# Optimization experiments

Measured on AMD Instinct MI355X. Metric: run time of the kernel, lower is better.

Reference implementation:

```python
import jax, jax.numpy as jnp
import numpy as np

N = 50000   # nodes
E = 600000  # edges
D = 128     # node_features (EvolveGCNO in=out channels)
H = 128     # hidden_dim (final Linear out)


def setup_inputs() -> dict:
    key = jax.random.key(0)
    ks = jax.random.split(key, 9)
    stdv = 1.0 / np.sqrt(D)
    u = lambda k, shape: jax.random.uniform(k, shape, jnp.float32, -stdv, stdv)
    return {
        "x": jax.random.normal(ks[0], (N, D), jnp.float32),
        "edge_index": jax.random.randint(ks[1], (2, E), 0, N),
        "edge_weight": jax.random.uniform(ks[2], (E,), jnp.float32),
        "W0": u(ks[3], (D, D)),        # EvolveGCNO initial_weight (squeezed)
        "w_ih": u(ks[4], (3 * D, D)),  # GRU input weights (r|z|n)
        "w_hh": u(ks[5], (3 * D, D)),  # GRU hidden weights (r|z|n)
        "b_ih": u(ks[6], (3 * D,)),
        "b_hh": u(ks[7], (3 * D,)),
        "W_lin": u(ks[8], (H, D)),     # torch Linear weight [out, in]
        "b_lin": jnp.zeros((H,), jnp.float32),
    }


def _gru_step(x, h, w_ih, w_hh, b_ih, b_hh):
    # One torch.nn.GRU cell step; here x == h == W0 (weight evolution).
    gi = x @ w_ih.T + b_ih
    gh = h @ w_hh.T + b_hh
    i_r, i_z, i_n = jnp.split(gi, 3, axis=-1)
    h_r, h_z, h_n = jnp.split(gh, 3, axis=-1)
    r = jax.nn.sigmoid(i_r + h_r)
    z = jax.nn.sigmoid(i_z + h_z)
    n = jnp.tanh(i_n + r * h_n)
    return (1.0 - z) * n + z * h


def reference(x, edge_index, edge_weight, W0, w_ih, w_hh, b_ih, b_hh, W_lin, b_lin):
    # 1) Evolve the GCN weight with one GRU step (input = hidden = W0).
    W = _gru_step(W0, W0, w_ih, w_hh, b_ih, b_hh)  # [D, D]

    # 2) GCNConv_Fixed_W: add self-loops (weight 1), symmetric normalization.
    loops = jnp.arange(N)
    row = jnp.concatenate([edge_index[0], loops])  # source
    col = jnp.concatenate([edge_index[1], loops])  # target
    ew = jnp.concatenate([edge_weight, jnp.ones((N,), x.dtype)])
    deg = jax.ops.segment_sum(ew, col, num_segments=N)
    dinv = jnp.where(deg > 0, jax.lax.rsqrt(deg), 0.0)
    norm = dinv[row] * ew * dinv[col]  # [E+N]

    xw = x @ W                                        # [N, D]
    h = jax.ops.segment_sum(norm[:, None] * xw[row], col, num_segments=N)  # [N, D]

    # 3) ReLU + Linear
    h = jax.nn.relu(h)
    return h @ W_lin.T + b_lin  # [N, H]
```

## Files before the change

kernel.cpp:

```cpp
#include <hip/hip_runtime.h>
#include <hip/hip_bf16.h>

#define NN 50000
#define EE 600000
#define DD 128
#define CAP 48
#define CNT_SHIFT 25
#define SUM_MASK 0x1FFFFFFu

typedef __attribute__((ext_vector_type(8))) __bf16 bf16x8;
typedef __attribute__((ext_vector_type(8))) short short8;
typedef __attribute__((ext_vector_type(4))) float f32x4;

__device__ __forceinline__ unsigned short f2bf(float f) {
    union { float f; unsigned u; } c; c.f = f;
    unsigned r = (c.u + 0x7fffu + ((c.u >> 16) & 1u)) >> 16;
    return (unsigned short)r;
}
__device__ __forceinline__ float bflo(unsigned u) {
    union { unsigned u; float f; } c; c.u = u << 16; return c.f;
}
__device__ __forceinline__ float bfhi(unsigned u) {
    union { unsigned u; float f; } c; c.u = u & 0xffff0000u; return c.f;
}
__device__ __forceinline__ float degof(unsigned p) {
    return 1.0f + (float)(p & SUM_MASK) * (1.0f / 65536.0f);
}

__global__ __launch_bounds__(256) void init_kernel(
    unsigned* __restrict__ cnt32,
    const float* __restrict__ W0, const float* __restrict__ w_ih,
    const float* __restrict__ w_hh, const float* __restrict__ b_ih,
    const float* __restrict__ b_hh, unsigned short* __restrict__ Wbt,
    const float* __restrict__ x, short* __restrict__ xb)
{
    if (blockIdx.x >= 113) {
        int u = (blockIdx.x - 113) * 256 + threadIdx.x;
        if (u < NN * DD / 8) {
            const float4* p = (const float4*)x + (size_t)u * 2;
            float4 f0 = p[0], f1 = p[1];
            short8 v;
            v[0] = (short)f2bf(f0.x); v[1] = (short)f2bf(f0.y);
            v[2] = (short)f2bf(f0.z); v[3] = (short)f2bf(f0.w);
            v[4] = (short)f2bf(f1.x); v[5] = (short)f2bf(f1.y);
            v[6] = (short)f2bf(f1.z); v[7] = (short)f2bf(f1.w);
            *(short8*)(xb + (size_t)u * 8) = v;
        }
        return;
    }
    if (blockIdx.x < 49) {
        int i = blockIdx.x * 256 + threadIdx.x;
        if (i < 50176 * 4 / 16) ((uint4*)cnt32)[i] = make_uint4(0u, 0u, 0u, 0u);
        return;
    }
    int idx = (blockIdx.x - 49) * 256 + threadIdx.x;
    int i = idx >> 7, j = idx & 127;
    const float4* a  = (const float4*)(W0  + i * DD);
    const float4* pr = (const float4*)(w_ih + (j        ) * DD);
    const float4* pz = (const float4*)(w_ih + (j + 128  ) * DD);
    const float4* pn = (const float4*)(w_ih + (j + 256  ) * DD);
    const float4* qr = (const float4*)(w_hh + (j        ) * DD);
    const float4* qz = (const float4*)(w_hh + (j + 128  ) * DD);
    const float4* qn = (const float4*)(w_hh + (j + 256  ) * DD);
    float ir = 0.f, iz = 0.f, inn = 0.f, hr = 0.f, hz = 0.f, hn = 0.f;
    for (int d = 0; d < DD / 4; ++d) {
        float4 av = a[d];
        float4 t;
        t = pr[d]; ir  += av.x*t.x + av.y*t.y + av.z*t.z + av.w*t.w;
        t = pz[d]; iz  += av.x*t.x + av.y*t.y + av.z*t.z + av.w*t.w;
        t = pn[d]; inn += av.x*t.x + av.y*t.y + av.z*t.z + av.w*t.w;
        t = qr[d]; hr  += av.x*t.x + av.y*t.y + av.z*t.z + av.w*t.w;
        t = qz[d]; hz  += av.x*t.x + av.y*t.y + av.z*t.z + av.w*t.w;
        t = qn[d]; hn  += av.x*t.x + av.y*t.y + av.z*t.z + av.w*t.w;
    }
    ir += b_ih[j]; iz += b_ih[j + 128]; inn += b_ih[j + 256];
    hr += b_hh[j]; hz += b_hh[j + 128]; hn  += b_hh[j + 256];
    float r = 1.f / (1.f + expf(-(ir + hr)));
    float z = 1.f / (1.f + expf(-(iz + hz)));
    float n = tanhf(inn + r * hn);
    float w = (1.f - z) * n + z * W0[idx];
    Wbt[j * DD + i] = f2bf(w);
}

__global__ __launch_bounds__(256) void histfill_kernel(
    const int* __restrict__ row, const int* __restrict__ col,
    const float* __restrict__ ew,
    unsigned* __restrict__ cnt32, unsigned* __restrict__ edges)
{
    int e = blockIdx.x * 256 + threadIdx.x;
    if (e >= EE) return;
    int c = col[e];
    unsigned wq = (unsigned)(ew[e] * 65536.0f);
    if (wq > 65535u) wq = 65535u;
    unsigned old = atomicAdd(&cnt32[c], (1u << CNT_SHIFT) | wq);
    unsigned oldcnt = old >> CNT_SHIFT;
    if (oldcnt < CAP)
        edges[(size_t)c * CAP + oldcnt] = (unsigned)row[e] | (wq << 16);
}

__global__ __launch_bounds__(256) void gather_kernel(
    const unsigned* __restrict__ edges, const unsigned* __restrict__ cnt32,
    const unsigned* __restrict__ xbu, unsigned* __restrict__ aggu)
{
    int wid  = threadIdx.x >> 6;
    int lane = threadIdx.x & 63;
    int node = blockIdx.x * 4 + wid;
    if (node >= NN) return;
    unsigned pn = cnt32[node];
    int n = (int)(pn >> CNT_SHIFT); if (n > CAP) n = CAP;
    const unsigned* eb = edges + (size_t)node * CAP;
    float s = rsqrtf(degof(pn));
    unsigned xs = xbu[(size_t)node * 64 + lane];
    float ax = s * bflo(xs), ay = s * bfhi(xs);
    int k = 0;
    int n8 = n & ~7;
    for (; k < n8; k += 8) {
        uint4 ra = *(const uint4*)(eb + k);
        uint4 rb = *(const uint4*)(eb + k + 4);
        int s0 = (int)(ra.x & 0xFFFFu), s1 = (int)(ra.y & 0xFFFFu);
        int s2 = (int)(ra.z & 0xFFFFu), s3 = (int)(ra.w & 0xFFFFu);
        int s4 = (int)(rb.x & 0xFFFFu), s5 = (int)(rb.y & 0xFFFFu);
        int s6 = (int)(rb.z & 0xFFFFu), s7 = (int)(rb.w & 0xFFFFu);
        unsigned p0 = cnt32[s0], p1 = cnt32[s1], p2 = cnt32[s2], p3 = cnt32[s3];
        unsigned p4 = cnt32[s4], p5 = cnt32[s5], p6 = cnt32[s6], p7 = cnt32[s7];
        unsigned x0 = xbu[(size_t)s0 * 64 + lane];
        unsigned x1 = xbu[(size_t)s1 * 64 + lane];
        unsigned x2 = xbu[(size_t)s2 * 64 + lane];
        unsigned x3 = xbu[(size_t)s3 * 64 + lane];
        unsigned x4 = xbu[(size_t)s4 * 64 + lane];
        unsigned x5 = xbu[(size_t)s5 * 64 + lane];
        unsigned x6 = xbu[(size_t)s6 * 64 + lane];
        unsigned x7 = xbu[(size_t)s7 * 64 + lane];
        float v0 = (float)(ra.x >> 16) * (1.0f / 65536.0f) * rsqrtf(degof(p0));
        float v1 = (float)(ra.y >> 16) * (1.0f / 65536.0f) * rsqrtf(degof(p1));
        float v2 = (float)(ra.z >> 16) * (1.0f / 65536.0f) * rsqrtf(degof(p2));
        float v3 = (float)(ra.w >> 16) * (1.0f / 65536.0f) * rsqrtf(degof(p3));
        float v4 = (float)(rb.x >> 16) * (1.0f / 65536.0f) * rsqrtf(degof(p4));
        float v5 = (float)(rb.y >> 16) * (1.0f / 65536.0f) * rsqrtf(degof(p5));
        float v6 = (float)(rb.z >> 16) * (1.0f / 65536.0f) * rsqrtf(degof(p6));
        float v7 = (float)(rb.w >> 16) * (1.0f / 65536.0f) * rsqrtf(degof(p7));
        ax += v0 * bflo(x0) + v1 * bflo(x1) + v2 * bflo(x2) + v3 * bflo(x3)
            + v4 * bflo(x4) + v5 * bflo(x5) + v6 * bflo(x6) + v7 * bflo(x7);
        ay += v0 * bfhi(x0) + v1 * bfhi(x1) + v2 * bfhi(x2) + v3 * bfhi(x3)
            + v4 * bfhi(x4) + v5 * bfhi(x5) + v6 * bfhi(x6) + v7 * bfhi(x7);
    }
    int n4 = n & ~3;
    for (; k < n4; k += 4) {
        uint4 rc = *(const uint4*)(eb + k);
        int s0 = (int)(rc.x & 0xFFFFu), s1 = (int)(rc.y & 0xFFFFu);
        int s2 = (int)(rc.z & 0xFFFFu), s3 = (int)(rc.w & 0xFFFFu);
        unsigned p0 = cnt32[s0], p1 = cnt32[s1], p2 = cnt32[s2], p3 = cnt32[s3];
        unsigned x0 = xbu[(size_t)s0 * 64 + lane];
        unsigned x1 = xbu[(size_t)s1 * 64 + lane];
        unsigned x2 = xbu[(size_t)s2 * 64 + lane];
        unsigned x3 = xbu[(size_t)s3 * 64 + lane];
        float v0 = (float)(rc.x >> 16) * (1.0f / 65536.0f) * rsqrtf(degof(p0));
        float v1 = (float)(rc.y >> 16) * (1.0f / 65536.0f) * rsqrtf(degof(p1));
        float v2 = (float)(rc.z >> 16) * (1.0f / 65536.0f) * rsqrtf(degof(p2));
        float v3 = (float)(rc.w >> 16) * (1.0f / 65536.0f) * rsqrtf(degof(p3));
        ax += v0 * bflo(x0) + v1 * bflo(x1) + v2 * bflo(x2) + v3 * bflo(x3);
        ay += v0 * bfhi(x0) + v1 * bfhi(x1) + v2 * bfhi(x2) + v3 * bfhi(x3);
    }
    for (; k < n; ++k) {
        unsigned r0 = eb[k];
        int s0 = (int)(r0 & 0xFFFFu);
        unsigned p0 = cnt32[s0];
        unsigned x0 = xbu[(size_t)s0 * 64 + lane];
        float v0 = (float)(r0 >> 16) * (1.0f / 65536.0f) * rsqrtf(degof(p0));
        ax += v0 * bflo(x0); ay += v0 * bfhi(x0);
    }
    aggu[(size_t)node * 64 + lane] =
        (unsigned)f2bf(ax * s) | ((unsigned)f2bf(ay * s) << 16);
}

__global__ __launch_bounds__(256) void fused_gemm(
    const short* __restrict__ agg, const short* __restrict__ Wbt,
    const float* __restrict__ Wlin, const float* __restrict__ bias,
    float* __restrict__ out)
{
    __shared__ __align__(16) short Bs1[DD * DD];
    __shared__ __align__(16) short Bs2[DD * DD];
    __shared__ __align__(16) short As[64 * DD];
    const int t = threadIdx.x;
    const int i0 = blockIdx.x * 64;

    for (int u = t; u < 2048; u += 256) {
        int byte = u << 4;
        int brow = byte >> 8;
        *(short8*)((char*)Bs1 + (byte ^ ((brow & 7) << 4))) =
            *(const short8*)((const char*)Wbt + byte);
    }
    for (int u = t; u < 2048; u += 256) {
        int brow = u >> 4;
        int kc = (u & 15) << 3;
        const float4* p = (const float4*)(Wlin + brow * DD + kc);
        float4 f0 = p[0], f1 = p[1];
        short8 v;
        v[0] = (short)f2bf(f0.x); v[1] = (short)f2bf(f0.y);
        v[2] = (short)f2bf(f0.z); v[3] = (short)f2bf(f0.w);
        v[4] = (short)f2bf(f1.x); v[5] = (short)f2bf(f1.y);
        v[6] = (short)f2bf(f1.z); v[7] = (short)f2bf(f1.w);
        int byte = (brow << 8) + (kc << 1);
        *(short8*)((char*)Bs2 + (byte ^ ((brow & 7) << 4))) = v;
    }
    for (int u = t; u < 1024; u += 256) {
        int arow = u >> 4;
        int kc = (u & 15) << 3;
        int grow = i0 + arow;
        short8 v;
#pragma unroll
        for (int i = 0; i < 8; ++i) v[i] = 0;
        if (grow < NN)
            v = *(const short8*)(agg + (size_t)grow * DD + kc);
        int byte = (arow << 8) + (kc << 1);
        *(short8*)((char*)As + (byte ^ ((arow & 7) << 4))) = v;
    }
    __syncthreads();

    const int lane = t & 63, wv = t >> 6;
    const int c0 = lane & 15, g = lane >> 4;
    const int arow = wv * 16 + c0;
    f32x4 acc[8];
#pragma unroll
    for (int n = 0; n < 8; ++n) { acc[n][0] = acc[n][1] = acc[n][2] = acc[n][3] = 0.f; }

#pragma unroll
    for (int s = 0; s < 4; ++s) {
        int k0 = s * 32 + g * 8;
        int abyte = (arow << 8) + (k0 << 1);
        bf16x8 a = *(const bf16x8*)((const char*)As + (abyte ^ ((arow & 7) << 4)));
#pragma unroll
        for (int n = 0; n < 8; ++n) {
            int bcol = n * 16 + c0;
            int bbyte = (bcol << 8) + (k0 << 1);
            bf16x8 b = *(const bf16x8*)((const char*)Bs1 + (bbyte ^ ((bcol & 7) << 4)));
            acc[n] = __builtin_amdgcn_mfma_f32_16x16x32_bf16(a, b, acc[n], 0, 0, 0);
        }
    }
    __syncthreads();

#pragma unroll
    for (int n = 0; n < 8; ++n) {
        int ccol = n * 16 + c0;
#pragma unroll
        for (int r = 0; r < 4; ++r) {
            int hrow = wv * 16 + g * 4 + r;
            int byte = (hrow << 8) + (ccol << 1);
            *(unsigned short*)((char*)As + (byte ^ ((hrow & 7) << 4))) =
                f2bf(fmaxf(acc[n][r], 0.f));
        }
    }
    __syncthreads();

#pragma unroll
    for (int n = 0; n < 8; ++n) { acc[n][0] = acc[n][1] = acc[n][2] = acc[n][3] = 0.f; }

#pragma unroll
    for (int s = 0; s < 4; ++s) {
        int k0 = s * 32 + g * 8;
        int abyte = (arow << 8) + (k0 << 1);
        bf16x8 a = *(const bf16x8*)((const char*)As + (abyte ^ ((arow & 7) << 4)));
#pragma unroll
        for (int n = 0; n < 8; ++n) {
            int bcol = n * 16 + c0;
            int bbyte = (bcol << 8) + (k0 << 1);
            bf16x8 b = *(const bf16x8*)((const char*)Bs2 + (bbyte ^ ((bcol & 7) << 4)));
            acc[n] = __builtin_amdgcn_mfma_f32_16x16x32_bf16(a, b, acc[n], 0, 0, 0);
        }
    }

#pragma unroll
    for (int n = 0; n < 8; ++n) {
        int ccol = n * 16 + c0;
        float bb = bias[ccol];
#pragma unroll
        for (int r = 0; r < 4; ++r) {
            int grow = i0 + wv * 16 + g * 4 + r;
            if (grow < NN)
                out[(size_t)grow * DD + ccol] = acc[n][r] + bb;
        }
    }
}

extern "C" void kernel_launch(void* const* d_in, const int* in_sizes, int n_in,
                              void* d_out, int out_size, void* d_ws, size_t ws_size,
                              hipStream_t stream)
{
    const float* x    = (const float*)d_in[0];
    const int*   ei   = (const int*)d_in[1];
    const float* ew   = (const float*)d_in[2];
    const float* W0   = (const float*)d_in[3];
    const float* w_ih = (const float*)d_in[4];
    const float* w_hh = (const float*)d_in[5];
    const float* b_ih = (const float*)d_in[6];
    const float* b_hh = (const float*)d_in[7];
    const float* Wlin = (const float*)d_in[8];
    const float* blin = (const float*)d_in[9];
    float* out = (float*)d_out;

    const int* row = ei;
    const int* col = ei + EE;

    char* ws = (char*)d_ws;
    unsigned short* Wbt = (unsigned short*)ws;
    unsigned* cnt32 = (unsigned*)(ws + 32768);
    short* xb   = (short*)(ws + 233472);
    short* agg  = (short*)(ws + 13033472);
    unsigned* edges = (unsigned*)(ws + 25833472);

    init_kernel<<<3238, 256, 0, stream>>>(cnt32, W0, w_ih, w_hh, b_ih, b_hh, Wbt, x, xb);

    histfill_kernel<<<(EE + 255) / 256, 256, 0, stream>>>(row, col, ew, cnt32, edges);

    gather_kernel<<<(NN + 3) / 4, 256, 0, stream>>>(
        edges, cnt32, (const unsigned*)xb, (unsigned*)agg);

    fused_gemm<<<(NN + 63) / 64, 256, 0, stream>>>(
        agg, (const short*)Wbt, Wlin, blin, out);
}
```

Measured before the change: 121.2 us.

## Fuse neighbor gather into the GEMM kernel via shared memory

Merges the gather aggregation kernel into the fused GEMM: each wave aggregates 16 nodes directly into the shared-memory A tile instead of writing an intermediate bf16 buffer to global memory. This removes the intermediate write/read and one kernel launch. In exchange the latency-bound gather now runs at much lower occupancy (few large-LDS blocks, serial nodes per wave), which may reduce latency hiding.

Result: slower. 174.3 us (+43.8%).

```diff
diff --git a/kernel.cpp b/kernel.cpp
--- a/kernel.cpp
+++ b/kernel.cpp
@@ -98,83 +98,9 @@
         edges[(size_t)c * CAP + oldcnt] = (unsigned)row[e] | (wq << 16);
 }
 
-__global__ __launch_bounds__(256) void gather_kernel(
+__global__ __launch_bounds__(256) void gather_gemm(
     const unsigned* __restrict__ edges, const unsigned* __restrict__ cnt32,
-    const unsigned* __restrict__ xbu, unsigned* __restrict__ aggu)
-{
-    int wid  = threadIdx.x >> 6;
-    int lane = threadIdx.x & 63;
-    int node = blockIdx.x * 4 + wid;
-    if (node >= NN) return;
-    unsigned pn = cnt32[node];
-    int n = (int)(pn >> CNT_SHIFT); if (n > CAP) n = CAP;
-    const unsigned* eb = edges + (size_t)node * CAP;
-    float s = rsqrtf(degof(pn));
-    unsigned xs = xbu[(size_t)node * 64 + lane];
-    float ax = s * bflo(xs), ay = s * bfhi(xs);
-    int k = 0;
-    int n8 = n & ~7;
-    for (; k < n8; k += 8) {
-        uint4 ra = *(const uint4*)(eb + k);
-        uint4 rb = *(const uint4*)(eb + k + 4);
-        int s0 = (int)(ra.x & 0xFFFFu), s1 = (int)(ra.y & 0xFFFFu);
-        int s2 = (int)(ra.z & 0xFFFFu), s3 = (int)(ra.w & 0xFFFFu);
-        int s4 = (int)(rb.x & 0xFFFFu), s5 = (int)(rb.y & 0xFFFFu);
-        int s6 = (int)(rb.z & 0xFFFFu), s7 = (int)(rb.w & 0xFFFFu);
-        unsigned p0 = cnt32[s0], p1 = cnt32[s1], p2 = cnt32[s2], p3 = cnt32[s3];
-        unsigned p4 = cnt32[s4], p5 = cnt32[s5], p6 = cnt32[s6], p7 = cnt32[s7];
-        unsigned x0 = xbu[(size_t)s0 * 64 + lane];
-        unsigned x1 = xbu[(size_t)s1 * 64 + lane];
-        unsigned x2 = xbu[(size_t)s2 * 64 + lane];
-        unsigned x3 = xbu[(size_t)s3 * 64 + lane];
-        unsigned x4 = xbu[(size_t)s4 * 64 + lane];
-        unsigned x5 = xbu[(size_t)s5 * 64 + lane];
-        unsigned x6 = xbu[(size_t)s6 * 64 + lane];
-        unsigned x7 = xbu[(size_t)s7 * 64 + lane];
-        float v0 = (float)(ra.x >> 16) * (1.0f / 65536.0f) * rsqrtf(degof(p0));
-        float v1 = (float)(ra.y >> 16) * (1.0f / 65536.0f) * rsqrtf(degof(p1));
-        float v2 = (float)(ra.z >> 16) * (1.0f / 65536.0f) * rsqrtf(degof(p2));
-        float v3 = (float)(ra.w >> 16) * (1.0f / 65536.0f) * rsqrtf(degof(p3));
-        float v4 = (float)(rb.x >> 16) * (1.0f / 65536.0f) * rsqrtf(degof(p4));
-        float v5 = (float)(rb.y >> 16) * (1.0f / 65536.0f) * rsqrtf(degof(p5));
-        float v6 = (float)(rb.z >> 16) * (1.0f / 65536.0f) * rsqrtf(degof(p6));
-        float v7 = (float)(rb.w >> 16) * (1.0f / 65536.0f) * rsqrtf(degof(p7));
-        ax += v0 * bflo(x0) + v1 * bflo(x1) + v2 * bflo(x2) + v3 * bflo(x3)
-            + v4 * bflo(x4) + v5 * bflo(x5) + v6 * bflo(x6) + v7 * bflo(x7);
-        ay += v0 * bfhi(x0) + v1 * bfhi(x1) + v2 * bfhi(x2) + v3 * bfhi(x3)
-            + v4 * bfhi(x4) + v5 * bfhi(x5) + v6 * bfhi(x6) + v7 * bfhi(x7);
-    }
-    int n4 = n & ~3;
-    for (; k < n4; k += 4) {
-        uint4 rc = *(const uint4*)(eb + k);
-        int s0 = (int)(rc.x & 0xFFFFu), s1 = (int)(rc.y & 0xFFFFu);
-        int s2 = (int)(rc.z & 0xFFFFu), s3 = (int)(rc.w & 0xFFFFu);
-        unsigned p0 = cnt32[s0], p1 = cnt32[s1], p2 = cnt32[s2], p3 = cnt32[s3];
-        unsigned x0 = xbu[(size_t)s0 * 64 + lane];
-        unsigned x1 = xbu[(size_t)s1 * 64 + lane];
-        unsigned x2 = xbu[(size_t)s2 * 64 + lane];
-        unsigned x3 = xbu[(size_t)s3 * 64 + lane];
-        float v0 = (float)(rc.x >> 16) * (1.0f / 65536.0f) * rsqrtf(degof(p0));
-        float v1 = (float)(rc.y >> 16) * (1.0f / 65536.0f) * rsqrtf(degof(p1));
-        float v2 = (float)(rc.z >> 16) * (1.0f / 65536.0f) * rsqrtf(degof(p2));
-        float v3 = (float)(rc.w >> 16) * (1.0f / 65536.0f) * rsqrtf(degof(p3));
-        ax += v0 * bflo(x0) + v1 * bflo(x1) + v2 * bflo(x2) + v3 * bflo(x3);
-        ay += v0 * bfhi(x0) + v1 * bfhi(x1) + v2 * bfhi(x2) + v3 * bfhi(x3);
-    }
-    for (; k < n; ++k) {
-        unsigned r0 = eb[k];
-        int s0 = (int)(r0 & 0xFFFFu);
-        unsigned p0 = cnt32[s0];
-        unsigned x0 = xbu[(size_t)s0 * 64 + lane];
-        float v0 = (float)(r0 >> 16) * (1.0f / 65536.0f) * rsqrtf(degof(p0));
-        ax += v0 * bflo(x0); ay += v0 * bfhi(x0);
-    }
-    aggu[(size_t)node * 64 + lane] =
-        (unsigned)f2bf(ax * s) | ((unsigned)f2bf(ay * s) << 16);
-}
-
-__global__ __launch_bounds__(256) void fused_gemm(
-    const short* __restrict__ agg, const short* __restrict__ Wbt,
+    const unsigned* __restrict__ xbu, const short* __restrict__ Wbt,
     const float* __restrict__ Wlin, const float* __restrict__ bias,
     float* __restrict__ out)
 {
@@ -183,6 +109,7 @@
     __shared__ __align__(16) short As[64 * DD];
     const int t = threadIdx.x;
     const int i0 = blockIdx.x * 64;
+    const int lane = t & 63, wv = t >> 6;
 
     for (int u = t; u < 2048; u += 256) {
         int byte = u << 4;
@@ -203,21 +130,82 @@
         int byte = (brow << 8) + (kc << 1);
         *(short8*)((char*)Bs2 + (byte ^ ((brow & 7) << 4))) = v;
     }
-    for (int u = t; u < 1024; u += 256) {
-        int arow = u >> 4;
-        int kc = (u & 15) << 3;
-        int grow = i0 + arow;
-        short8 v;
-#pragma unroll
-        for (int i = 0; i < 8; ++i) v[i] = 0;
-        if (grow < NN)
-            v = *(const short8*)(agg + (size_t)grow * DD + kc);
-        int byte = (arow << 8) + (kc << 1);
-        *(short8*)((char*)As + (byte ^ ((arow & 7) << 4))) = v;
+
+    for (int ni = 0; ni < 16; ++ni) {
+        int arow = wv * 16 + ni;
+        int node = i0 + arow;
+        unsigned val = 0u;
+        if (node < NN) {
+            unsigned pn = cnt32[node];
+            int n = (int)(pn >> CNT_SHIFT); if (n > CAP) n = CAP;
+            const unsigned* eb = edges + (size_t)node * CAP;
+            float s = rsqrtf(degof(pn));
+            unsigned xs = xbu[(size_t)node * 64 + lane];
+            float ax = s * bflo(xs), ay = s * bfhi(xs);
+            int k = 0;
+            int n8 = n & ~7;
+            for (; k < n8; k += 8) {
+                uint4 ra = *(const uint4*)(eb + k);
+                uint4 rb = *(const uint4*)(eb + k + 4);
+                int s0 = (int)(ra.x & 0xFFFFu), s1 = (int)(ra.y & 0xFFFFu);
+                int s2 = (int)(ra.z & 0xFFFFu), s3 = (int)(ra.w & 0xFFFFu);
+                int s4 = (int)(rb.x & 0xFFFFu), s5 = (int)(rb.y & 0xFFFFu);
+                int s6 = (int)(rb.z & 0xFFFFu), s7 = (int)(rb.w & 0xFFFFu);
+                unsigned p0 = cnt32[s0], p1 = cnt32[s1], p2 = cnt32[s2], p3 = cnt32[s3];
+                unsigned p4 = cnt32[s4], p5 = cnt32[s5], p6 = cnt32[s6], p7 = cnt32[s7];
+                unsigned x0 = xbu[(size_t)s0 * 64 + lane];
+                unsigned x1 = xbu[(size_t)s1 * 64 + lane];
+                unsigned x2 = xbu[(size_t)s2 * 64 + lane];
+                unsigned x3 = xbu[(size_t)s3 * 64 + lane];
+                unsigned x4 = xbu[(size_t)s4 * 64 + lane];
+                unsigned x5 = xbu[(size_t)s5 * 64 + lane];
+                unsigned x6 = xbu[(size_t)s6 * 64 + lane];
+                unsigned x7 = xbu[(size_t)s7 * 64 + lane];
+                float v0 = (float)(ra.x >> 16) * (1.0f / 65536.0f) * rsqrtf(degof(p0));
+                float v1 = (float)(ra.y >> 16) * (1.0f / 65536.0f) * rsqrtf(degof(p1));
+                float v2 = (float)(ra.z >> 16) * (1.0f / 65536.0f) * rsqrtf(degof(p2));
+                float v3 = (float)(ra.w >> 16) * (1.0f / 65536.0f) * rsqrtf(degof(p3));
+                float v4 = (float)(rb.x >> 16) * (1.0f / 65536.0f) * rsqrtf(degof(p4));
+                float v5 = (float)(rb.y >> 16) * (1.0f / 65536.0f) * rsqrtf(degof(p5));
+                float v6 = (float)(rb.z >> 16) * (1.0f / 65536.0f) * rsqrtf(degof(p6));
+                float v7 = (float)(rb.w >> 16) * (1.0f / 65536.0f) * rsqrtf(degof(p7));
+                ax += v0 * bflo(x0) + v1 * bflo(x1) + v2 * bflo(x2) + v3 * bflo(x3)
+                    + v4 * bflo(x4) + v5 * bflo(x5) + v6 * bflo(x6) + v7 * bflo(x7);
+                ay += v0 * bfhi(x0) + v1 * bfhi(x1) + v2 * bfhi(x2) + v3 * bfhi(x3)
+                    + v4 * bfhi(x4) + v5 * bfhi(x5) + v6 * bfhi(x6) + v7 * bfhi(x7);
+            }
+            int n4 = n & ~3;
+            for (; k < n4; k += 4) {
+                uint4 rc = *(const uint4*)(eb + k);
+                int s0 = (int)(rc.x & 0xFFFFu), s1 = (int)(rc.y & 0xFFFFu);
+                int s2 = (int)(rc.z & 0xFFFFu), s3 = (int)(rc.w & 0xFFFFu);
+                unsigned p0 = cnt32[s0], p1 = cnt32[s1], p2 = cnt32[s2], p3 = cnt32[s3];
+                unsigned x0 = xbu[(size_t)s0 * 64 + lane];
+                unsigned x1 = xbu[(size_t)s1 * 64 + lane];
+                unsigned x2 = xbu[(size_t)s2 * 64 + lane];
+                unsigned x3 = xbu[(size_t)s3 * 64 + lane];
+                float v0 = (float)(rc.x >> 16) * (1.0f / 65536.0f) * rsqrtf(degof(p0));
+                float v1 = (float)(rc.y >> 16) * (1.0f / 65536.0f) * rsqrtf(degof(p1));
+                float v2 = (float)(rc.z >> 16) * (1.0f / 65536.0f) * rsqrtf(degof(p2));
+                float v3 = (float)(rc.w >> 16) * (1.0f / 65536.0f) * rsqrtf(degof(p3));
+                ax += v0 * bflo(x0) + v1 * bflo(x1) + v2 * bflo(x2) + v3 * bflo(x3);
+                ay += v0 * bfhi(x0) + v1 * bfhi(x1) + v2 * bfhi(x2) + v3 * bfhi(x3);
+            }
+            for (; k < n; ++k) {
+                unsigned r0 = eb[k];
+                int s0 = (int)(r0 & 0xFFFFu);
+                unsigned p0 = cnt32[s0];
+                unsigned x0 = xbu[(size_t)s0 * 64 + lane];
+                float v0 = (float)(r0 >> 16) * (1.0f / 65536.0f) * rsqrtf(degof(p0));
+                ax += v0 * bflo(x0); ay += v0 * bfhi(x0);
+            }
+            val = (unsigned)f2bf(ax * s) | ((unsigned)f2bf(ay * s) << 16);
+        }
+        int byte = (arow << 8) + (lane << 2);
+        *(unsigned*)((char*)As + (byte ^ ((arow & 7) << 4))) = val;
     }
     __syncthreads();
 
-    const int lane = t & 63, wv = t >> 6;
     const int c0 = lane & 15, g = lane >> 4;
     const int arow = wv * 16 + c0;
     f32x4 acc[8];
@@ -305,16 +293,12 @@
     unsigned short* Wbt = (unsigned short*)ws;
     unsigned* cnt32 = (unsigned*)(ws + 32768);
     short* xb   = (short*)(ws + 233472);
-    short* agg  = (short*)(ws + 13033472);
-    unsigned* edges = (unsigned*)(ws + 25833472);
+    unsigned* edges = (unsigned*)(ws + 13033472);
 
     init_kernel<<<3238, 256, 0, stream>>>(cnt32, W0, w_ih, w_hh, b_ih, b_hh, Wbt, x, xb);
 
     histfill_kernel<<<(EE + 255) / 256, 256, 0, stream>>>(row, col, ew, cnt32, edges);
 
-    gather_kernel<<<(NN + 3) / 4, 256, 0, stream>>>(
-        edges, cnt32, (const unsigned*)xb, (unsigned*)agg);
-
-    fused_gemm<<<(NN + 63) / 64, 256, 0, stream>>>(
-        agg, (const short*)Wbt, Wlin, blin, out);
-}
+    gather_gemm<<<(NN + 63) / 64, 256, 0, stream>>>(
+        edges, cnt32, (const unsigned*)xb, (const short*)Wbt, Wlin, blin, out);
+}
```
